# Performance work log

Hardware: AMD Instinct MI355X
Metric: run time of the kernel (lower is better)

## Reference

```python
import jax, jax.numpy as jnp
import numpy as np
from jax import lax

R, K = 1000, 80                 # proposals per image, foreground classes
IMG_H, IMG_W = 800.0, 1333.0    # image_shape (h, w) used by Boxes.clip
SCORE_THRESH = 0.05
NMS_THRESH = 0.5
TOPK = 100                      # topk_per_image


def setup_inputs() -> dict:
    key = jax.random.key(0)
    k1, k2, k3 = jax.random.split(key, 3)
    # well-formed class-specific boxes: x1y1 + positive wh
    x1y1 = jax.random.uniform(k1, (R, K, 2)) * jnp.array([IMG_W - 60.0, IMG_H - 60.0])
    wh = jax.random.uniform(k2, (R, K, 2)) * 200.0 + 10.0
    boxes = jnp.concatenate([x1y1, x1y1 + wh], axis=-1).reshape(R, K * 4)
    logits = jax.random.normal(k3, (R, K + 1)) * 2.0
    scores = jax.nn.softmax(logits, axis=-1)  # (R, K+1), last col = background
    return {"boxes": boxes, "scores": scores}


def _iou_matrix(b):
    # b: [R, 4] (x1, y1, x2, y2) -> [R, R] pairwise IoU
    x1, y1, x2, y2 = b[:, 0], b[:, 1], b[:, 2], b[:, 3]
    area = jnp.clip(x2 - x1, 0.0) * jnp.clip(y2 - y1, 0.0)
    xx1 = jnp.maximum(x1[:, None], x1[None, :])
    yy1 = jnp.maximum(y1[:, None], y1[None, :])
    xx2 = jnp.minimum(x2[:, None], x2[None, :])
    yy2 = jnp.minimum(y2[:, None], y2[None, :])
    inter = jnp.clip(xx2 - xx1, 0.0) * jnp.clip(yy2 - yy1, 0.0)
    union = area[:, None] + area[None, :] - inter
    return inter / jnp.maximum(union, 1e-9)


def _nms_one_class(boxes_c, scores_c, valid_c):
    # boxes_c: [R,4], scores_c: [R], valid_c: [R] bool (passed score filter)
    masked = jnp.where(valid_c, scores_c, -jnp.inf)
    order = jnp.argsort(-masked)            # descending score
    b = boxes_c[order]
    s = masked[order]
    v = valid_c[order]
    iou = iou_full = _iou_matrix(b)          # [R, R]
    idx = jnp.arange(R)

    def body(i, keep):
        # box i (if still kept & valid) suppresses later boxes with high IoU
        sup = (iou_full[i] > NMS_THRESH) & keep[i] & (idx > i)
        return keep & ~sup

    keep = lax.fori_loop(0, R, body, v)
    return s, keep, order


def reference(boxes, scores):
    # boxes: (R, K*4), scores: (R, K+1)
    bx = boxes.reshape(R, K, 4)
    # Boxes.clip(image_shape=(h, w)): x in [0, w], y in [0, h]
    bx = jnp.stack([
        jnp.clip(bx[..., 0], 0.0, IMG_W),
        jnp.clip(bx[..., 1], 0.0, IMG_H),
        jnp.clip(bx[..., 2], 0.0, IMG_W),
        jnp.clip(bx[..., 3], 0.0, IMG_H),
    ], axis=-1)

    fg = scores[:, :-1]                                  # (R, K) foreground scores
    thres = jnp.minimum(SCORE_THRESH, (fg.mean() + fg.max()) / 2.0)
    valid = fg > thres                                   # filter_mask

    # per-class batched NMS (equivalent to torchvision batched_nms)
    boxes_k = jnp.transpose(bx, (1, 0, 2))               # [K, R, 4]
    s_sorted, keep, order = jax.vmap(_nms_one_class)(boxes_k, fg.T, valid.T)

    flat = jnp.where(keep, s_sorted, -jnp.inf).reshape(-1)   # [K*R]
    topv, topi = lax.top_k(flat, TOPK)                   # keep[:topk], score-sorted
    cls = topi // R
    pos = topi % R
    prop = order[cls, pos]                               # original proposal index (filter_inds[:,0])
    ok = jnp.isfinite(topv)
    okf = ok.astype(boxes.dtype)

    box_out = bx[prop, cls] * okf[:, None]               # pred_boxes  [TOPK, 4]
    sc_out = jnp.where(ok, topv, 0.0)                    # scores      [TOPK]
    full_out = scores[prop] * okf[:, None]               # full_scores [TOPK, K+1]
    cls_out = (cls * ok).astype(boxes.dtype)             # pred_classes as float col

    # packed result: [boxes(4) | score(1) | class(1) | full_scores(K+1)]
    return jnp.concatenate([box_out, sc_out[:, None], cls_out[:, None], full_out], axis=1)
```

## Files before the change

kernel.cpp:

```cpp
#include <hip/hip_runtime.h>
#include <stdint.h>

typedef unsigned long long u64;
typedef unsigned int u32;

#define R_N 1000
#define K_N 80
#define NCOL 81
#define TOPK_N 100
#define OUT_W 87
#define IMG_W_ 1333.0f
#define IMG_H_ 800.0f
#define CSTR 100
#define CSTRP 101
#define NQUAD ((R_N * NCOL) / 4)
#define NMAX 448
#define WMAX 7
#define KM (K_N * CSTR)
#define POISON 0xAAAAAAAAu

__device__ __forceinline__ u32 f32_order(float f) {
    u32 u = __float_as_uint(f);
    return u ^ (((u32)((int)u >> 31)) | 0x80000000u);
}
__device__ __forceinline__ float f32_unorder(u32 o) {
    u32 u = (o & 0x80000000u) ? (o ^ 0x80000000u) : ~o;
    return __uint_as_float(u);
}

__device__ __forceinline__ void grid_barrier(u32* bar, u32 nblk) {
    __syncthreads();
    if (threadIdx.x == 0) {
        __threadfence();
        if (__hip_atomic_load(bar, __ATOMIC_RELAXED, __HIP_MEMORY_SCOPE_AGENT) == POISON)
            atomicCAS(bar, POISON, 0u);
        __hip_atomic_fetch_add(bar, 1u, __ATOMIC_ACQ_REL, __HIP_MEMORY_SCOPE_AGENT);
        while (__hip_atomic_load(bar, __ATOMIC_ACQUIRE, __HIP_MEMORY_SCOPE_AGENT) < nblk)
            __builtin_amdgcn_s_sleep(2);
    }
    __syncthreads();
}

struct P2 {
    float4 bx4[R_N];
    u64 key_s[R_N];
    u64 pool[NMAX * WMAX];
    float area[R_N];
    float sc[R_N];
    u64 keep_words[16];
    int s_n;
};
struct P3 {
    u64 keys[K_N * CSTRP];
    int rnk[TOPK_N];
};
union SMEM { P2 p2; P3 p3; };

__global__ __launch_bounds__(256, 1) void k_all(const float* __restrict__ boxes,
                                                const float* __restrict__ scores,
                                                float* __restrict__ hdr,
                                                u32* __restrict__ bars,
                                                u64* __restrict__ cand,
                                                float* __restrict__ outp) {
    __shared__ SMEM sm;
    __shared__ float s_sum[4], s_max[4];
    __shared__ int s_cnt[4], s_kb[2];
    __shared__ float s_thres;

    const int bid = blockIdx.x, tid = threadIdx.x;
    const int lane = tid & 63, wv = tid >> 6;
    const int c = bid;
    const u64 below = (lane == 0) ? 0ull : (~0ull >> (64 - lane));

    for (int r = tid; r < R_N; r += 256) sm.p2.sc[r] = scores[r * NCOL + c];

    {
        float sum = 0.f, mx = -1e30f;
        int q = bid * 256 + tid;
        if (q < NQUAD) {
            float4 v = ((const float4*)scores)[q];
            int m = (q * 4) % NCOL;
            float vv[4] = {v.x, v.y, v.z, v.w};
#pragma unroll
            for (int e = 0; e < 4; ++e) {
                int mm = m + e; if (mm >= NCOL) mm -= NCOL;
                if (mm != K_N) { sum += vv[e]; mx = fmaxf(mx, vv[e]); }
            }
        }
#pragma unroll
        for (int off = 32; off > 0; off >>= 1) {
            sum += __shfl_down(sum, off);
            mx = fmaxf(mx, __shfl_down(mx, off));
        }
        if (lane == 0) { s_sum[wv] = sum; s_max[wv] = mx; }
        __syncthreads();
        if (tid == 0) {
            hdr[2 * bid] = s_sum[0] + s_sum[1] + s_sum[2] + s_sum[3];
            hdr[2 * bid + 1] = fmaxf(fmaxf(s_max[0], s_max[1]), fmaxf(s_max[2], s_max[3]));
        }
    }

    float th = 0.05f;
    for (int pass = 0; ; ++pass) {
        u64* ukey = sm.p2.pool;
        if (wv == 0) {
            int nn = 0;
            for (int r0 = 0; r0 < R_N; r0 += 64) {
                int r = r0 + lane;
                bool pred = (r < R_N) && (sm.p2.sc[r] > th);
                u64 m = __ballot(pred);
                if (pred) {
                    int slot = nn + __popcll(m & below);
                    ukey[slot] = ((u64)f32_order(sm.p2.sc[r]) << 32) | (u64)(u32)(R_N - 1 - r);
                }
                nn += __popcll(m);
            }
            if (lane == 0) sm.p2.s_n = nn;
        }
        __syncthreads();
        const int n = sm.p2.s_n;

        for (int j = tid; j < n; j += 256) {
            u64 kj = ukey[j];
            int rank = 0;
            for (int k = 0; k < n; ++k) rank += (ukey[k] > kj) ? 1 : 0;
            int r = (R_N - 1) - (int)(kj & 0xFFFFFFFFull);
            float4 b = ((const float4*)boxes)[r * K_N + c];
            float x1 = fminf(fmaxf(b.x, 0.f), IMG_W_);
            float y1 = fminf(fmaxf(b.y, 0.f), IMG_H_);
            float x2 = fminf(fmaxf(b.z, 0.f), IMG_W_);
            float y2 = fminf(fmaxf(b.w, 0.f), IMG_H_);
            sm.p2.key_s[rank] = kj;
            sm.p2.bx4[rank] = make_float4(x1, y1, x2, y2);
            sm.p2.area[rank] = fmaxf(x2 - x1, 0.f) * fmaxf(y2 - y1, 0.f);
        }
        __syncthreads();

        if (n <= NMAX) {
            const int W = (n + 63) >> 6;
            u64* Mrow = sm.p2.pool;
            const int nh = n >> 1;
            for (int t2 = wv; t2 < 2 * W; t2 += 4) {
                int w = t2 >> 1, ih = t2 & 1;
                int i0 = ih ? nh : 0;
                int i1 = ih ? n : nh;
                int j = w * 64 + lane;
                bool jv = j < n;
                float4 bj = jv ? sm.p2.bx4[j] : make_float4(0.f, 0.f, 0.f, 0.f);
                float aj = jv ? sm.p2.area[j] : 0.f;
                for (int i = i0; i < i1; ++i) {
                    float4 bi = sm.p2.bx4[i];
                    float ai = sm.p2.area[i];
                    float xx1 = fmaxf(bi.x, bj.x), yy1 = fmaxf(bi.y, bj.y);
                    float xx2 = fminf(bi.z, bj.z), yy2 = fminf(bi.w, bj.w);
                    float inter = fmaxf(xx2 - xx1, 0.f) * fmaxf(yy2 - yy1, 0.f);
                    bool sup = jv && (j > i) &&
                               (inter / fmaxf(ai + aj - inter, 1e-9f) > 0.5f);
                    u64 m = __ballot(sup);
                    if (lane == 0) Mrow[i * W + w] = m;
                }
            }
            __syncthreads();

            if (wv == 0) {
                u64 keep_w = 0;
                if (lane < W) {
                    int rem = n - lane * 64;
                    keep_w = (rem >= 64) ? ~0ull : ((1ull << rem) - 1ull);
                }
                const int lw = (lane < W) ? lane : 0;
                u64 fifo[8];
#pragma unroll
                for (int d = 0; d < 8; ++d) fifo[d] = (d < n) ? Mrow[d * W + lw] : 0ull;
                for (int ib = 0; ib < n; ib += 8) {
#pragma unroll
                    for (int d = 0; d < 8; ++d) {
                        int i = ib + d;
                        if (i >= n) break;
                        u64 row = fifo[d];
                        int ip = i + 8;
                        fifo[d] = (ip < n) ? Mrow[ip * W + lw] : 0ull;
                        u64 kw = __shfl(keep_w, i >> 6);
                        if ((kw >> (i & 63)) & 1ull) keep_w &= ~row;
                    }
                }
                if (lane < W) sm.p2.keep_words[lane] = keep_w;
                if (lane >= W && lane < 16) sm.p2.keep_words[lane] = 0;
            }
        } else {
            int* keep = (int*)sm.p2.pool;
            for (int j = tid; j < n; j += 256) keep[j] = 1;
            __syncthreads();
            for (int i = 0; i < n - 1; ++i) {
                __syncthreads();
                if (!keep[i]) continue;
                float4 bi = sm.p2.bx4[i];
                float ai = sm.p2.area[i];
                for (int j = i + 1 + tid; j < n; j += 256) {
                    if (!keep[j]) continue;
                    float xx1 = fmaxf(bi.x, sm.p2.bx4[j].x), yy1 = fmaxf(bi.y, sm.p2.bx4[j].y);
                    float xx2 = fminf(bi.z, sm.p2.bx4[j].z), yy2 = fminf(bi.w, sm.p2.bx4[j].w);
                    float inter = fmaxf(xx2 - xx1, 0.f) * fmaxf(yy2 - yy1, 0.f);
                    if (inter / fmaxf(ai + sm.p2.area[j] - inter, 1e-9f) > 0.5f) keep[j] = 0;
                }
            }
            __syncthreads();
            if (wv == 0) {
                for (int w = 0; w < 16; ++w) {
                    int j = w * 64 + lane;
                    u64 m = __ballot((j < n) && keep[j]);
                    if (lane == 0) sm.p2.keep_words[w] = m;
                }
            }
        }
        __syncthreads();

        if (wv == 0) {
            int kb = 0;
            for (int j0 = 0; j0 < n; j0 += 64) {
                int j = j0 + lane;
                u64 mw = sm.p2.keep_words[j0 >> 6];
                bool kp = (j < n) && ((mw >> lane) & 1ull);
                u64 mm = __ballot(kp);
                int kr = kb + __popcll(mm & below);
                if (kp && kr < CSTR) {
                    u64 kj = sm.p2.key_s[j];
                    u32 osc = (u32)(kj >> 32);
                    int rr = (R_N - 1) - (int)(kj & 0xFFFFFFFFull);
                    int flat = c * R_N + j;
                    cand[c * CSTR + kr] =
                        ((u64)osc << 27) | ((u64)(u32)(131071 - flat) << 10) | (u64)(u32)rr;
                }
                kb += __popcll(mm);
            }
            if (kb > CSTR) kb = CSTR;
            for (int k2 = kb + lane; k2 < CSTR; k2 += 64) cand[c * CSTR + k2] = 0;
        }

        if (pass == 0) {
            grid_barrier(&bars[0], K_N);
            if (wv == 0) {
                float S = hdr[2 * lane], M = hdr[2 * lane + 1];
                if (lane + 64 < K_N) {
                    S += hdr[2 * (lane + 64)];
                    M = fmaxf(M, hdr[2 * (lane + 64) + 1]);
                }
#pragma unroll
                for (int off = 32; off > 0; off >>= 1) {
                    S += __shfl_down(S, off);
                    M = fmaxf(M, __shfl_down(M, off));
                }
                if (lane == 0)
                    s_thres = fminf(0.05f, 0.5f * (S / (float)(R_N * K_N) + M));
            }
            __syncthreads();
            if (s_thres == 0.05f) break;
            th = s_thres;
        } else {
            grid_barrier(&bars[1], K_N);
            break;
        }
    }

    {
        const ulonglong2* cp = (const ulonglong2*)cand;
        int cnt = 0;
        for (int t = tid; t < KM / 2; t += 256) {
            ulonglong2 v = cp[t];
            int e0 = 2 * t;
            int cc = e0 / CSTR, pos = e0 - cc * CSTR;
            sm.p3.keys[cc * CSTRP + pos] = v.x;
            sm.p3.keys[cc * CSTRP + pos + 1] = v.y;
            cnt += (v.x != 0ull) + (v.y != 0ull);
        }
#pragma unroll
        for (int off = 32; off > 0; off >>= 1) cnt += __shfl_down(cnt, off);
        if (lane == 0) s_cnt[wv] = cnt;
        if (tid < TOPK_N) sm.p3.rnk[tid] = tid;
        __syncthreads();
        const int total = s_cnt[0] + s_cnt[1] + s_cnt[2] + s_cnt[3];
        const int target = total < TOPK_N ? total : TOPK_N;

        if (wv < 2) {
            int t = wv * 64 + lane;
            bool nz = (t < CSTR) && (sm.p3.keys[c * CSTRP + t] != 0ull);
            u64 m = __ballot(nz);
            if (lane == 0) s_kb[wv] = __popcll(m);
        }
        __syncthreads();
        const int kb = s_kb[0] + s_kb[1];

        const int TASKS = kb * (K_N - 1);
        for (int g = 0; g * 2048 < TASKS; ++g) {
            int lo[8], hi[8], ii[8], base[8];
            u64 xv[8];
            bool act[8];
#pragma unroll
            for (int s = 0; s < 8; ++s) {
                int t = g * 2048 + s * 256 + tid;
                act[s] = t < TASKS;
                int i = 0, cc = 0;
                if (act[s]) { i = t % kb; cc = t / kb; }
                cc += (cc >= c);
                ii[s] = i;
                base[s] = cc * CSTRP;
                xv[s] = sm.p3.keys[c * CSTRP + i];
                if (xv[s] == 0ull) act[s] = false;
                lo[s] = 0; hi[s] = CSTR;
            }
#pragma unroll
            for (int st = 0; st < 7; ++st) {
#pragma unroll
                for (int s = 0; s < 8; ++s) {
                    int mid = (lo[s] + hi[s]) >> 1;
                    u64 v = sm.p3.keys[base[s] + mid];
                    bool live = lo[s] < hi[s];
                    bool gt = live && (v > xv[s]);
                    lo[s] = gt ? mid + 1 : lo[s];
                    hi[s] = (live && !gt) ? mid : hi[s];
                }
            }
#pragma unroll
            for (int s = 0; s < 8; ++s)
                if (act[s] && lo[s] > 0) atomicAdd(&sm.p3.rnk[ii[s]], lo[s]);
        }
        __syncthreads();

        if (tid < CSTR) {
            u64 x = sm.p3.keys[c * CSTRP + tid];
            int r = sm.p3.rnk[tid];
            if (x != 0ull && r < target) {
                int prop = (int)(x & 0x3FFull);
                float score = f32_unorder((u32)((x >> 27) & 0xFFFFFFFFull));
                int ob = r * OUT_W;
                float4 bx = ((const float4*)boxes)[prop * K_N + c];
                outp[ob + 0] = fminf(fmaxf(bx.x, 0.f), IMG_W_);
                outp[ob + 1] = fminf(fmaxf(bx.y, 0.f), IMG_H_);
                outp[ob + 2] = fminf(fmaxf(bx.z, 0.f), IMG_W_);
                outp[ob + 3] = fminf(fmaxf(bx.w, 0.f), IMG_H_);
                outp[ob + 4] = score;
                outp[ob + 5] = (float)c;
                const int sb = prop * NCOL;
#pragma unroll 9
                for (int j = 0; j < NCOL; ++j) outp[ob + 6 + j] = scores[sb + j];
            }
        }
        for (int row = target + bid; row < TOPK_N; row += K_N) {
            int ob = row * OUT_W;
            for (int e = tid; e < OUT_W; e += 256) outp[ob + e] = 0.f;
        }
    }
}

extern "C" void kernel_launch(void* const* d_in, const int* in_sizes, int n_in,
                              void* d_out, int out_size, void* d_ws, size_t ws_size,
                              hipStream_t stream) {
    const float* boxes = (const float*)d_in[0];
    const float* scores = (const float*)d_in[1];
    float* hdr = (float*)d_ws;
    u32* bars = (u32*)((char*)d_ws + 768);
    u64* cand = (u64*)((char*)d_ws + 1024);

    k_all<<<dim3(K_N), dim3(256), 0, stream>>>(boxes, scores, hdr, bars, cand, (float*)d_out);
}
```

Baseline: 101.7 us.

## Load candidates right after each grid barrier and parallelize output row writes

```diff
diff --git a/kernel.cpp b/kernel.cpp
--- a/kernel.cpp
+++ b/kernel.cpp
@@ -46,13 +46,15 @@
     u64 key_s[R_N];
     u64 pool[NMAX * WMAX];
     float area[R_N];
-    float sc[R_N];
     u64 keep_words[16];
     int s_n;
 };
 struct P3 {
     u64 keys[K_N * CSTRP];
     int rnk[TOPK_N];
+    u64 wx[TOPK_N];
+    int wr[TOPK_N];
+    int wn;
 };
 union SMEM { P2 p2; P3 p3; };
 
@@ -63,6 +65,7 @@
                                                 u64* __restrict__ cand,
                                                 float* __restrict__ outp) {
     __shared__ SMEM sm;
+    __shared__ float sc[R_N];
     __shared__ float s_sum[4], s_max[4];
     __shared__ int s_cnt[4], s_kb[2];
     __shared__ float s_thres;
@@ -72,7 +75,7 @@
     const int c = bid;
     const u64 below = (lane == 0) ? 0ull : (~0ull >> (64 - lane));
 
-    for (int r = tid; r < R_N; r += 256) sm.p2.sc[r] = scores[r * NCOL + c];
+    for (int r = tid; r < R_N; r += 256) sc[r] = scores[r * NCOL + c];
 
     {
         float sum = 0.f, mx = -1e30f;
@@ -107,11 +110,11 @@
             int nn = 0;
             for (int r0 = 0; r0 < R_N; r0 += 64) {
                 int r = r0 + lane;
-                bool pred = (r < R_N) && (sm.p2.sc[r] > th);
+                bool pred = (r < R_N) && (sc[r] > th);
                 u64 m = __ballot(pred);
                 if (pred) {
                     int slot = nn + __popcll(m & below);
-                    ukey[slot] = ((u64)f32_order(sm.p2.sc[r]) << 32) | (u64)(u32)(R_N - 1 - r);
+                    ukey[slot] = ((u64)f32_order(sc[r]) << 32) | (u64)(u32)(R_N - 1 - r);
                 }
                 nn += __popcll(m);
             }
@@ -237,8 +240,25 @@
             for (int k2 = kb + lane; k2 < CSTR; k2 += 64) cand[c * CSTR + k2] = 0;
         }
 
+        grid_barrier(&bars[pass], K_N);
+
+        {
+            const ulonglong2* cp = (const ulonglong2*)cand;
+            int cnt = 0;
+            for (int t = tid; t < KM / 2; t += 256) {
+                ulonglong2 v = cp[t];
+                int e0 = 2 * t;
+                int cc2 = e0 / CSTR, pos = e0 - cc2 * CSTR;
+                sm.p3.keys[cc2 * CSTRP + pos] = v.x;
+                sm.p3.keys[cc2 * CSTRP + pos + 1] = v.y;
+                cnt += (v.x != 0ull) + (v.y != 0ull);
+            }
+#pragma unroll
+            for (int off = 32; off > 0; off >>= 1) cnt += __shfl_down(cnt, off);
+            if (lane == 0) s_cnt[wv] = cnt;
+        }
+
         if (pass == 0) {
-            grid_barrier(&bars[0], K_N);
             if (wv == 0) {
                 float S = hdr[2 * lane], M = hdr[2 * lane + 1];
                 if (lane + 64 < K_N) {
@@ -256,31 +276,16 @@
             __syncthreads();
             if (s_thres == 0.05f) break;
             th = s_thres;
-        } else {
-            grid_barrier(&bars[1], K_N);
-            break;
-        }
+        } else break;
     }
 
     {
-        const ulonglong2* cp = (const ulonglong2*)cand;
-        int cnt = 0;
-        for (int t = tid; t < KM / 2; t += 256) {
-            ulonglong2 v = cp[t];
-            int e0 = 2 * t;
-            int cc = e0 / CSTR, pos = e0 - cc * CSTR;
-            sm.p3.keys[cc * CSTRP + pos] = v.x;
-            sm.p3.keys[cc * CSTRP + pos + 1] = v.y;
-            cnt += (v.x != 0ull) + (v.y != 0ull);
-        }
-#pragma unroll
-        for (int off = 32; off > 0; off >>= 1) cnt += __shfl_down(cnt, off);
-        if (lane == 0) s_cnt[wv] = cnt;
-        if (tid < TOPK_N) sm.p3.rnk[tid] = tid;
         __syncthreads();
         const int total = s_cnt[0] + s_cnt[1] + s_cnt[2] + s_cnt[3];
         const int target = total < TOPK_N ? total : TOPK_N;
 
+        if (tid < TOPK_N) sm.p3.rnk[tid] = tid;
+        if (tid == 0) sm.p3.wn = 0;
         if (wv < 2) {
             int t = wv * 64 + lane;
             bool nz = (t < CSTR) && (sm.p3.keys[c * CSTRP + t] != 0ull);
@@ -299,11 +304,11 @@
             for (int s = 0; s < 8; ++s) {
                 int t = g * 2048 + s * 256 + tid;
                 act[s] = t < TASKS;
-                int i = 0, cc = 0;
-                if (act[s]) { i = t % kb; cc = t / kb; }
-                cc += (cc >= c);
+                int i = 0, cc2 = 0;
+                if (act[s]) { i = t % kb; cc2 = t / kb; }
+                cc2 += (cc2 >= c);
                 ii[s] = i;
-                base[s] = cc * CSTRP;
+                base[s] = cc2 * CSTRP;
                 xv[s] = sm.p3.keys[c * CSTRP + i];
                 if (xv[s] == 0ull) act[s] = false;
                 lo[s] = 0; hi[s] = CSTR;
@@ -326,24 +331,35 @@
         }
         __syncthreads();
 
-        if (tid < CSTR) {
-            u64 x = sm.p3.keys[c * CSTRP + tid];
+        if (tid < kb) {
             int r = sm.p3.rnk[tid];
-            if (x != 0ull && r < target) {
-                int prop = (int)(x & 0x3FFull);
-                float score = f32_unorder((u32)((x >> 27) & 0xFFFFFFFFull));
-                int ob = r * OUT_W;
-                float4 bx = ((const float4*)boxes)[prop * K_N + c];
-                outp[ob + 0] = fminf(fmaxf(bx.x, 0.f), IMG_W_);
-                outp[ob + 1] = fminf(fmaxf(bx.y, 0.f), IMG_H_);
-                outp[ob + 2] = fminf(fmaxf(bx.z, 0.f), IMG_W_);
-                outp[ob + 3] = fminf(fmaxf(bx.w, 0.f), IMG_H_);
-                outp[ob + 4] = score;
-                outp[ob + 5] = (float)c;
-                const int sb = prop * NCOL;
-#pragma unroll 9
-                for (int j = 0; j < NCOL; ++j) outp[ob + 6 + j] = scores[sb + j];
-            }
+            if (r < target) {
+                int idx = atomicAdd(&sm.p3.wn, 1);
+                sm.p3.wx[idx] = sm.p3.keys[c * CSTRP + tid];
+                sm.p3.wr[idx] = r;
+            }
+        }
+        __syncthreads();
+        const int wn = sm.p3.wn;
+
+        for (int e = tid; e < wn * OUT_W; e += 256) {
+            int w = e / OUT_W, col = e - w * OUT_W;
+            u64 x = sm.p3.wx[w];
+            int r = sm.p3.wr[w];
+            int prop = (int)(x & 0x3FFull);
+            float val;
+            if (col < 4) {
+                float b = boxes[prop * (K_N * 4) + c * 4 + col];
+                float lim = (col & 1) ? IMG_H_ : IMG_W_;
+                val = fminf(fmaxf(b, 0.f), lim);
+            } else if (col == 4) {
+                val = f32_unorder((u32)((x >> 27) & 0xFFFFFFFFull));
+            } else if (col == 5) {
+                val = (float)c;
+            } else {
+                val = scores[prop * NCOL + (col - 6)];
+            }
+            outp[r * OUT_W + col] = val;
         }
         for (int row = target + bid; row < TOPK_N; row += K_N) {
             int ob = row * OUT_W;
```

After: 100.6 us. About the same (-1.1%).
